# Performance work log

Measured on AMD Instinct MI355X. Metric: run time of the kernel, lower is better.

## Reference

```python
import jax, jax.numpy as jnp
import numpy as np

B, C, LQ, D = 4096, 64, 32, 128
H = 192  # 1.5 * dim
MARGIN = 1.0
EPS = 1e-12


def l2norm(x):
    return x * jax.lax.rsqrt(jnp.maximum(jnp.sum(x * x, axis=1, keepdims=True), EPS))


def setup_inputs() -> dict:
    key = jax.random.key(0)
    ks = jax.random.split(key, 16)
    question_word_embs = jax.random.normal(ks[0], (B, LQ, D), jnp.float32)
    question_lengths = jax.random.randint(ks[1], (B,), 1, LQ + 1, jnp.int32)
    header_embs = jax.random.normal(ks[2], (B, C, D), jnp.float32)
    table_word_embs = jax.random.normal(ks[3], (B, C, D), jnp.float32)
    num_cols = jax.random.randint(ks[4], (B,), 1, C + 1, jnp.int32)
    masks = (jnp.arange(C)[None, :] < num_cols[:, None]).astype(jnp.float32)
    labels = (jax.random.uniform(ks[5], (B,)) < 0.5).astype(jnp.float32)
    # table_encoder_dense: Dense(1.5*dim, relu) -> Dense(dim, relu)
    W1 = jax.random.normal(ks[6], (2 * D, H), jnp.float32) / np.sqrt(2 * D)
    b1 = jnp.zeros((H,), jnp.float32)
    W2 = jax.random.normal(ks[7], (H, D), jnp.float32) / np.sqrt(H)
    b2 = jnp.zeros((D,), jnp.float32)
    # query LSTM(dim, activation='relu'): gate order i, f, c, o (Keras)
    Wx = jax.random.normal(ks[8], (D, 4 * D), jnp.float32) / np.sqrt(D)
    Wh = jax.random.normal(ks[9], (D, 4 * D), jnp.float32) / np.sqrt(D)
    b_lstm = jnp.zeros((4 * D,), jnp.float32)
    return dict(question_word_embs=question_word_embs, question_lengths=question_lengths,
                header_embs=header_embs, table_word_embs=table_word_embs,
                num_cols=num_cols, masks=masks, labels=labels,
                W1=W1, b1=b1, W2=W2, b2=b2, Wx=Wx, Wh=Wh, b_lstm=b_lstm)


def masked_lstm(x, lengths, Wx, Wh, b):
    # x: [B, L, D]; returns final hidden state at each row's true length
    xs = jnp.transpose(x, (1, 0, 2))  # [L, B, D]
    h0 = jnp.zeros((x.shape[0], D), x.dtype)
    c0 = jnp.zeros_like(h0)

    def step(carry, inp):
        h, c = carry
        t, x_t = inp
        z = x_t @ Wx + h @ Wh + b  # [B, 4D]
        i, f, g, o = jnp.split(z, 4, axis=1)
        i = jax.nn.sigmoid(i)
        f = jax.nn.sigmoid(f)
        g = jax.nn.relu(g)           # activation='relu'
        o = jax.nn.sigmoid(o)
        c_new = f * c + i * g
        h_new = o * jax.nn.relu(c_new)
        m = (t < lengths)[:, None].astype(x_t.dtype)
        return (m * h_new + (1 - m) * h, m * c_new + (1 - m) * c), None

    (h, _), _ = jax.lax.scan(step, (h0, c0), (jnp.arange(xs.shape[0]), xs))
    return h


def reference(question_word_embs, question_lengths, header_embs, table_word_embs,
              num_cols, masks, labels, W1, b1, W2, b2, Wx, Wh, b_lstm):
    # ---- table path ----
    flat = jnp.concatenate([header_embs.reshape(-1, D), table_word_embs.reshape(-1, D)], axis=1)  # [B*C, 2D]
    h = jax.nn.relu(flat @ W1 + b1)
    te = jax.nn.relu(h @ W2 + b2).reshape(B, C, D)
    te = te * masks[:, :, None]
    te = jnp.sum(te, axis=1) / num_cols.astype(jnp.float32)[:, None]
    te = l2norm(te)
    # ---- query path (ragged-word LSTM encoder) ----
    qe = masked_lstm(question_word_embs, question_lengths, Wx, Wh, b_lstm)
    qe = l2norm(qe)
    # ---- contrastive loss ----
    d = jnp.sum(jnp.square(qe - te), axis=1)
    d_sqrt = jnp.sqrt(d)
    loss = labels * d + (1.0 - labels) * jnp.square(jnp.maximum(0.0, MARGIN - d_sqrt))
    return 0.5 * jnp.mean(loss)
```

## Files before the change

kernel.cpp:

```cpp
#include <hip/hip_runtime.h>
#include <math.h>

#define B_  4096
#define C_  64
#define LQ_ 32
#define D_  128
#define H_  192

typedef __attribute__((ext_vector_type(8))) short bf16x8;
typedef __attribute__((ext_vector_type(4))) float f32x4;

#define KEEP(x) asm volatile("" : "+v"(x))

__device__ inline unsigned cvt_pk_bf16(float lo, float hi) {
    unsigned r;
    asm("v_cvt_pk_bf16_f32 %0, %1, %2" : "=v"(r) : "v"(lo), "v"(hi));
    return r;
}
__device__ inline short f2b(float x) { return (short)(cvt_pk_bf16(x, x) & 0xffff); }
__device__ inline float sigm(float x) { return 1.f / (1.f + __expf(-x)); }

__device__ inline void wg_barrier() {
    asm volatile("s_waitcnt lgkmcnt(0)" ::: "memory");
    __builtin_amdgcn_s_barrier();
    asm volatile("" ::: "memory");
}

__global__ __launch_bounds__(256) void prep_kernel(
    const float* __restrict__ W1, const float* __restrict__ W2,
    const float* __restrict__ Wx, const float* __restrict__ Wh,
    short* __restrict__ W1T, short* __restrict__ W2T, short* __restrict__ WTl)
{
    int idx = blockIdx.x * 256 + threadIdx.x;
    if (idx < 192 * 256) {
        int j = idx >> 8, k = idx & 255;
        W1T[idx] = f2b(W1[k * H_ + j]);
    }
    if (idx < 128 * 192) {
        int j = idx / 192, k = idx - j * 192;
        W2T[idx] = f2b(W2[k * D_ + j]);
    }
    if (idx < 512 * 256) {
        int p = idx >> 8, k = idx & 255;
        int w = p >> 6, g = (p >> 4) & 3, jj = p & 15;
        int jo = g * 128 + w * 16 + jj;
        float v = (k < 128) ? Wx[k * 512 + jo] : Wh[(k - 128) * 512 + jo];
        WTl[idx] = f2b(v);
    }
}

__global__ __launch_bounds__(256, 2)
void table_kernel(
    const float* __restrict__ header, const float* __restrict__ tword,
    const float* __restrict__ masks, const int* __restrict__ num_cols,
    const short* __restrict__ W1T, const float* __restrict__ b1,
    const short* __restrict__ W2T, const float* __restrict__ b2,
    float* __restrict__ te_out)
{
    const int bb0 = blockIdx.x * 4;
    const int tid = threadIdx.x;
    const int w   = tid >> 6;
    const int l   = tid & 63;
    const int lg  = l >> 4;
    const int ln  = l & 15;

    __shared__ __align__(16) short flat_s[2][16 * 256];
    __shared__ __align__(16) short h_s[16 * 192];
    __shared__ float msk_s[4][64];
    __shared__ float ncol_s[4];
    __shared__ float redv[128];
    __shared__ float redq[2];

    bf16x8 bw1[3][8];
    float bias1[3][4];
    #pragma unroll
    for (int ct = 0; ct < 3; ++ct) {
        int j = w * 48 + ct * 16 + ln;
        #pragma unroll
        for (int ks = 0; ks < 8; ++ks)
            bw1[ct][ks] = *(const bf16x8*)&W1T[j * 256 + ks * 32 + lg * 8];
        #pragma unroll
        for (int reg = 0; reg < 4; ++reg)
            bias1[ct][reg] = b1[w * 48 + ct * 16 + lg * 4 + reg];
    }
    bf16x8 bw2[2][6];
    float bias2[2][4];
    #pragma unroll
    for (int ct = 0; ct < 2; ++ct) {
        int j = w * 32 + ct * 16 + ln;
        #pragma unroll
        for (int ks = 0; ks < 6; ++ks)
            bw2[ct][ks] = *(const bf16x8*)&W2T[j * 192 + ks * 32 + lg * 8];
        #pragma unroll
        for (int reg = 0; reg < 4; ++reg)
            bias2[ct][reg] = b2[w * 32 + ct * 16 + lg * 4 + reg];
    }
    #pragma unroll
    for (int ct = 0; ct < 3; ++ct) {
        #pragma unroll
        for (int ks = 0; ks < 8; ++ks) KEEP(bw1[ct][ks]);
        #pragma unroll
        for (int reg = 0; reg < 4; ++reg) KEEP(bias1[ct][reg]);
    }
    #pragma unroll
    for (int ct = 0; ct < 2; ++ct) {
        #pragma unroll
        for (int ks = 0; ks < 6; ++ks) KEEP(bw2[ct][ks]);
        #pragma unroll
        for (int reg = 0; reg < 4; ++reg) KEEP(bias2[ct][reg]);
    }

    ((float*)msk_s)[tid] = masks[(size_t)bb0 * C_ + tid];
    if (tid < 4) ncol_s[tid] = (float)num_cols[bb0 + tid];
    __syncthreads();

    float4 pf0[4], pf1[4];
    auto issue = [&](int cc, float4 (&dst)[4]) {
        int b    = bb0 + (cc >> 2);
        int row0 = (cc & 3) * 16;
        #pragma unroll
        for (int i = 0; i < 4; ++i) {
            int idx = i * 256 + tid;
            int r   = idx >> 6;
            int c   = idx & 63;
            const float* src = (c < 32)
                ? &header[((size_t)b * C_ + row0 + r) * D_ + c * 4]
                : &tword [((size_t)b * C_ + row0 + r) * D_ + (c - 32) * 4];
            dst[i] = *(const float4*)src;
        }
    };
    issue(0, pf0);
    issue(1, pf1);

    float csum[2][4] = {{0.f, 0.f, 0.f, 0.f}, {0.f, 0.f, 0.f, 0.f}};
    const int row = ln;
    const int swz = (ln & 7) << 4;

    auto body = [&](int cc, float4 (&pfc)[4], char* fbuf) {
        const int bi = cc >> 2;

        #pragma unroll
        for (int i = 0; i < 4; ++i) {
            int idx = i * 256 + tid;
            int r   = idx >> 6;
            int c   = idx & 63;
            uint2 p;
            p.x = cvt_pk_bf16(pfc[i].x, pfc[i].y);
            p.y = cvt_pk_bf16(pfc[i].z, pfc[i].w);
            *(uint2*)(fbuf + r * 512 + ((c * 8) ^ ((r & 7) << 4))) = p;
        }
        if (cc + 2 < 16) issue(cc + 2, pfc);
        wg_barrier();

        {
            f32x4 acc[3];
            #pragma unroll
            for (int ct = 0; ct < 3; ++ct)
                acc[ct] = (f32x4){bias1[ct][0], bias1[ct][1], bias1[ct][2], bias1[ct][3]};
            #pragma unroll
            for (int ks = 0; ks < 8; ++ks) {
                bf16x8 a = *(const bf16x8*)(fbuf + row * 512 + ((ks * 64 + lg * 16) ^ swz));
                #pragma unroll
                for (int ct = 0; ct < 3; ++ct)
                    acc[ct] = __builtin_amdgcn_mfma_f32_16x16x32_bf16(bw1[ct][ks], a, acc[ct], 0, 0, 0);
            }
            #pragma unroll
            for (int ct = 0; ct < 3; ++ct) {
                int col0 = w * 48 + ct * 16 + lg * 4;
                uint2 hp;
                hp.x = cvt_pk_bf16(fmaxf(acc[ct][0], 0.f), fmaxf(acc[ct][1], 0.f));
                hp.y = cvt_pk_bf16(fmaxf(acc[ct][2], 0.f), fmaxf(acc[ct][3], 0.f));
                *(uint2*)((char*)h_s + row * 384 + ((col0 * 2) ^ swz)) = hp;
            }
        }
        wg_barrier();

        {
            f32x4 acc2[2];
            #pragma unroll
            for (int ct = 0; ct < 2; ++ct)
                acc2[ct] = (f32x4){bias2[ct][0], bias2[ct][1], bias2[ct][2], bias2[ct][3]};
            #pragma unroll
            for (int ks = 0; ks < 6; ++ks) {
                bf16x8 a = *(const bf16x8*)((char*)h_s + row * 384 + ((ks * 64 + lg * 16) ^ swz));
                #pragma unroll
                for (int ct = 0; ct < 2; ++ct)
                    acc2[ct] = __builtin_amdgcn_mfma_f32_16x16x32_bf16(bw2[ct][ks], a, acc2[ct], 0, 0, 0);
            }
            float m = msk_s[bi][(cc & 3) * 16 + ln];
            #pragma unroll
            for (int ct = 0; ct < 2; ++ct)
                #pragma unroll
                for (int reg = 0; reg < 4; ++reg)
                    csum[ct][reg] = fmaf(fmaxf(acc2[ct][reg], 0.f), m, csum[ct][reg]);
        }

        if ((cc & 3) == 3) {
            #pragma unroll
            for (int s = 1; s < 16; s <<= 1)
                #pragma unroll
                for (int ct = 0; ct < 2; ++ct)
                    #pragma unroll
                    for (int reg = 0; reg < 4; ++reg)
                        csum[ct][reg] += __shfl_xor(csum[ct][reg], s, 64);
            if (ln == 0) {
                #pragma unroll
                for (int ct = 0; ct < 2; ++ct)
                    #pragma unroll
                    for (int reg = 0; reg < 4; ++reg)
                        redv[w * 32 + ct * 16 + lg * 4 + reg] = csum[ct][reg];
            }
            wg_barrier();
            float v = 0.f;
            if (tid < 128) {
                v = redv[tid] / ncol_s[bi];
                float s2 = v * v;
                #pragma unroll
                for (int sh = 1; sh < 64; sh <<= 1) s2 += __shfl_xor(s2, sh, 64);
                if (l == 0) redq[w] = s2;
            }
            wg_barrier();
            if (tid < 128) {
                float inv = rsqrtf(fmaxf(redq[0] + redq[1], 1e-12f));
                te_out[(size_t)(bb0 + bi) * D_ + tid] = v * inv;
            }
            #pragma unroll
            for (int ct = 0; ct < 2; ++ct)
                #pragma unroll
                for (int reg = 0; reg < 4; ++reg)
                    csum[ct][reg] = 0.f;
        }
    };

    for (int p = 0; p < 8; ++p) {
        body(p * 2,     pf0, (char*)flat_s[0]);
        body(p * 2 + 1, pf1, (char*)flat_s[1]);
    }
}

__global__ __launch_bounds__(512) __attribute__((amdgpu_waves_per_eu(1, 2)))
void lstm_kernel(
    const float* __restrict__ q, const int* __restrict__ lengths,
    const short* __restrict__ WTl, const float* __restrict__ bl,
    float* __restrict__ qe_out)
{
    const int tid = threadIdx.x;
    const int b0  = blockIdx.x * 16;
    const int w   = tid >> 6;
    const int l   = tid & 63;
    const int lg  = l >> 4;
    const int ln  = l & 15;
    const int d0  = w * 16 + lg * 4;

    __shared__ __align__(16) short xh[2][16 * 256];
    __shared__ float red8[8][16];

    bf16x8 wf[4][8];
    #pragma unroll
    for (int g = 0; g < 4; ++g)
        #pragma unroll
        for (int ks = 0; ks < 8; ++ks)
            wf[g][ks] = *(const bf16x8*)&WTl[(w * 64 + g * 16 + ln) * 256 + ks * 32 + lg * 8];
    float bias[4][4];
    #pragma unroll
    for (int g = 0; g < 4; ++g)
        #pragma unroll
        for (int reg = 0; reg < 4; ++reg)
            bias[g][reg] = bl[g * 128 + d0 + reg];
    #pragma unroll
    for (int g = 0; g < 4; ++g) {
        #pragma unroll
        for (int ks = 0; ks < 8; ++ks) KEEP(wf[g][ks]);
        #pragma unroll
        for (int reg = 0; reg < 4; ++reg) KEEP(bias[g][reg]);
    }

    float creg[4] = {0.f, 0.f, 0.f, 0.f};
    float hreg[4] = {0.f, 0.f, 0.f, 0.f};
    const int len = lengths[b0 + ln];
    const int sr = tid >> 5, sc = tid & 31;

    float4 qv = *(const float4*)&q[((size_t)(b0 + sr) * LQ_ + 0) * D_ + sc * 4];

    for (int t = 0; t < LQ_; ++t) {
        char* buf = (char*)xh[t & 1];
        uint2 px; px.x = cvt_pk_bf16(qv.x, qv.y); px.y = cvt_pk_bf16(qv.z, qv.w);
        *(uint2*)(buf + sr * 512 + ((sc * 8) ^ ((sr & 7) << 4))) = px;
        uint2 ph; ph.x = cvt_pk_bf16(hreg[0], hreg[1]); ph.y = cvt_pk_bf16(hreg[2], hreg[3]);
        *(uint2*)(buf + ln * 512 + ((256 + d0 * 2) ^ ((ln & 7) << 4))) = ph;
        if (t + 1 < LQ_)
            qv = *(const float4*)&q[((size_t)(b0 + sr) * LQ_ + (t + 1)) * D_ + sc * 4];
        wg_barrier();

        f32x4 acc[4];
        #pragma unroll
        for (int g = 0; g < 4; ++g)
            acc[g] = (f32x4){bias[g][0], bias[g][1], bias[g][2], bias[g][3]};
        #pragma unroll
        for (int ks = 0; ks < 8; ++ks) {
            bf16x8 xf = *(const bf16x8*)(buf + ln * 512 + ((ks * 64 + lg * 16) ^ ((ln & 7) << 4)));
            #pragma unroll
            for (int g = 0; g < 4; ++g)
                acc[g] = __builtin_amdgcn_mfma_f32_16x16x32_bf16(wf[g][ks], xf, acc[g], 0, 0, 0);
        }

        bool live = (t < len);
        #pragma unroll
        for (int reg = 0; reg < 4; ++reg) {
            float iv = sigm(acc[0][reg]);
            float fv = sigm(acc[1][reg]);
            float gv = fmaxf(acc[2][reg], 0.f);
            float ov = sigm(acc[3][reg]);
            float cn = fmaf(fv, creg[reg], iv * gv);
            float hn = ov * fmaxf(cn, 0.f);
            if (live) { creg[reg] = cn; hreg[reg] = hn; }
        }
    }

    float sq = 0.f;
    #pragma unroll
    for (int reg = 0; reg < 4; ++reg) sq = fmaf(hreg[reg], hreg[reg], sq);
    sq += __shfl_xor(sq, 16, 64);
    sq += __shfl_xor(sq, 32, 64);
    if (l < 16) red8[w][ln] = sq;
    wg_barrier();
    float tot = 0.f;
    #pragma unroll
    for (int ww = 0; ww < 8; ++ww) tot += red8[ww][ln];
    float inv = rsqrtf(fmaxf(tot, 1e-12f));
    float4 o;
    o.x = hreg[0] * inv; o.y = hreg[1] * inv; o.z = hreg[2] * inv; o.w = hreg[3] * inv;
    *(float4*)&qe_out[(size_t)(b0 + ln) * D_ + d0] = o;
}

__global__ __launch_bounds__(64) void loss_kernel(
    const float* __restrict__ te, const float* __restrict__ qe,
    const float* __restrict__ labels, float* __restrict__ partial)
{
    const int tid = threadIdx.x;
    const int b   = blockIdx.x * 64 + tid;
    float dsum = 0.f;
    #pragma unroll 8
    for (int k4 = 0; k4 < 32; ++k4) {
        float4 a = *(const float4*)&qe[(size_t)b * D_ + k4 * 4];
        float4 c = *(const float4*)&te[(size_t)b * D_ + k4 * 4];
        float dx = a.x - c.x, dy = a.y - c.y, dz = a.z - c.z, dw = a.w - c.w;
        dsum += dx * dx + dy * dy + dz * dz + dw * dw;
    }
    float lab = labels[b];
    float ds  = sqrtf(dsum);
    float ml  = fmaxf(0.f, 1.f - ds);
    float loss = lab * dsum + (1.f - lab) * ml * ml;
    #pragma unroll
    for (int s = 32; s > 0; s >>= 1) loss += __shfl_xor(loss, s, 64);
    if (tid == 0) partial[blockIdx.x] = loss;
}

__global__ void final_kernel(const float* __restrict__ partial, float* __restrict__ out)
{
    const int tid = threadIdx.x;
    float v = partial[tid];
    #pragma unroll
    for (int s = 32; s > 0; s >>= 1) v += __shfl_xor(v, s, 64);
    if (tid == 0) out[0] = 0.5f * v / (float)B_;
}

extern "C" void kernel_launch(void* const* d_in, const int* in_sizes, int n_in,
                              void* d_out, int out_size, void* d_ws, size_t ws_size,
                              hipStream_t stream)
{
    const float* q      = (const float*)d_in[0];
    const int*   qlen   = (const int*)d_in[1];
    const float* header = (const float*)d_in[2];
    const float* tword  = (const float*)d_in[3];
    const int*   ncols  = (const int*)d_in[4];
    const float* masks  = (const float*)d_in[5];
    const float* labels = (const float*)d_in[6];
    const float* W1     = (const float*)d_in[7];
    const float* b1     = (const float*)d_in[8];
    const float* W2     = (const float*)d_in[9];
    const float* b2     = (const float*)d_in[10];
    const float* Wx     = (const float*)d_in[11];
    const float* Wh     = (const float*)d_in[12];
    const float* bl     = (const float*)d_in[13];
    float* out = (float*)d_out;

    float* te      = (float*)d_ws;
    float* qe      = te + (size_t)B_ * D_;
    float* partial = qe + (size_t)B_ * D_;
    short* W1T     = (short*)(partial + 64);
    short* W2T     = W1T + 192 * 256;
    short* WTl     = W2T + 128 * 192;

    prep_kernel<<<512, 256, 0, stream>>>(W1, W2, Wx, Wh, W1T, W2T, WTl);
    table_kernel<<<B_ / 4, 256, 0, stream>>>(header, tword, masks, ncols, W1T, b1, W2T, b2, te);
    lstm_kernel<<<B_ / 16, 512, 0, stream>>>(q, qlen, WTl, bl, qe);
    loss_kernel<<<B_ / 64, 64, 0, stream>>>(te, qe, labels, partial);
    final_kernel<<<1, 64, 0, stream>>>(partial, out);
}
```

Measured before the change: 150.8 us.

## Double-buffer hidden tile and defer per-table normalization to cut barriers

The table kernel now double-buffers the hidden-activation tile in shared memory. Staging of the next input chunk moves between the two GEMM stages, so each chunk needs one fewer workgroup barrier. The per-batch reduction and L2 normalization, which used two extra barriers every four chunks, is deferred: partial column sums go into a per-batch shared array and all four batch rows are normalized once at the end. This uses more LDS and changes the prefetch ordering, which may affect occupancy at two blocks per CU.

Result: slower. 191.6 us (+27.1%).

```diff
diff --git a/kernel.cpp b/kernel.cpp
--- a/kernel.cpp
+++ b/kernel.cpp
@@ -65,11 +65,11 @@
     const int ln  = l & 15;
 
     __shared__ __align__(16) short flat_s[2][16 * 256];
-    __shared__ __align__(16) short h_s[16 * 192];
+    __shared__ __align__(16) short h_s2[2][16 * 192];
     __shared__ float msk_s[4][64];
     __shared__ float ncol_s[4];
-    __shared__ float redv[128];
-    __shared__ float redq[2];
+    __shared__ float csum_s[4][128];
+    __shared__ float redq[2][4];
 
     bf16x8 bw1[3][8];
     float bias1[3][4];
@@ -112,7 +112,6 @@
 
     ((float*)msk_s)[tid] = masks[(size_t)bb0 * C_ + tid];
     if (tid < 4) ncol_s[tid] = (float)num_cols[bb0 + tid];
-    __syncthreads();
 
     float4 pf0[4], pf1[4];
     auto issue = [&](int cc, float4 (&dst)[4]) {
@@ -129,16 +128,7 @@
             dst[i] = *(const float4*)src;
         }
     };
-    issue(0, pf0);
-    issue(1, pf1);
-
-    float csum[2][4] = {{0.f, 0.f, 0.f, 0.f}, {0.f, 0.f, 0.f, 0.f}};
-    const int row = ln;
-    const int swz = (ln & 7) << 4;
-
-    auto body = [&](int cc, float4 (&pfc)[4], char* fbuf) {
-        const int bi = cc >> 2;
-
+    auto stage = [&](float4 (&pfc)[4], char* fbuf) {
         #pragma unroll
         for (int i = 0; i < 4; ++i) {
             int idx = i * 256 + tid;
@@ -149,8 +139,24 @@
             p.y = cvt_pk_bf16(pfc[i].z, pfc[i].w);
             *(uint2*)(fbuf + r * 512 + ((c * 8) ^ ((r & 7) << 4))) = p;
         }
-        if (cc + 2 < 16) issue(cc + 2, pfc);
-        wg_barrier();
+    };
+
+    issue(0, pf0);
+    issue(1, pf1);
+    __syncthreads();
+
+    stage(pf0, (char*)flat_s[0]);
+    issue(2, pf0);
+    wg_barrier();
+
+    float csum[2][4] = {{0.f, 0.f, 0.f, 0.f}, {0.f, 0.f, 0.f, 0.f}};
+    const int row = ln;
+    const int swz = (ln & 7) << 4;
+
+    auto body = [&](int cc, float4 (&pfN)[4], bool doStage) {
+        char* fbuf = (char*)flat_s[cc & 1];
+        char* hbuf = (char*)h_s2[cc & 1];
+        const int bi = cc >> 2;
 
         {
             f32x4 acc[3];
@@ -170,9 +176,15 @@
                 uint2 hp;
                 hp.x = cvt_pk_bf16(fmaxf(acc[ct][0], 0.f), fmaxf(acc[ct][1], 0.f));
                 hp.y = cvt_pk_bf16(fmaxf(acc[ct][2], 0.f), fmaxf(acc[ct][3], 0.f));
-                *(uint2*)((char*)h_s + row * 384 + ((col0 * 2) ^ swz)) = hp;
+                *(uint2*)(hbuf + row * 384 + ((col0 * 2) ^ swz)) = hp;
             }
         }
+
+        if (doStage) {
+            stage(pfN, (char*)flat_s[(cc + 1) & 1]);
+            if (cc + 3 < 16) issue(cc + 3, pfN);
+        }
+
         wg_barrier();
 
         {
@@ -182,7 +194,7 @@
                 acc2[ct] = (f32x4){bias2[ct][0], bias2[ct][1], bias2[ct][2], bias2[ct][3]};
             #pragma unroll
             for (int ks = 0; ks < 6; ++ks) {
-                bf16x8 a = *(const bf16x8*)((char*)h_s + row * 384 + ((ks * 64 + lg * 16) ^ swz));
+                bf16x8 a = *(const bf16x8*)(hbuf + row * 384 + ((ks * 64 + lg * 16) ^ swz));
                 #pragma unroll
                 for (int ct = 0; ct < 2; ++ct)
                     acc2[ct] = __builtin_amdgcn_mfma_f32_16x16x32_bf16(bw2[ct][ks], a, acc2[ct], 0, 0, 0);
@@ -208,21 +220,7 @@
                 for (int ct = 0; ct < 2; ++ct)
                     #pragma unroll
                     for (int reg = 0; reg < 4; ++reg)
-                        redv[w * 32 + ct * 16 + lg * 4 + reg] = csum[ct][reg];
-            }
-            wg_barrier();
-            float v = 0.f;
-            if (tid < 128) {
-                v = redv[tid] / ncol_s[bi];
-                float s2 = v * v;
-                #pragma unroll
-                for (int sh = 1; sh < 64; sh <<= 1) s2 += __shfl_xor(s2, sh, 64);
-                if (l == 0) redq[w] = s2;
-            }
-            wg_barrier();
-            if (tid < 128) {
-                float inv = rsqrtf(fmaxf(redq[0] + redq[1], 1e-12f));
-                te_out[(size_t)(bb0 + bi) * D_ + tid] = v * inv;
+                        csum_s[bi][w * 32 + ct * 16 + lg * 4 + reg] = csum[ct][reg];
             }
             #pragma unroll
             for (int ct = 0; ct < 2; ++ct)
@@ -232,9 +230,32 @@
         }
     };
 
+    #pragma unroll 1
     for (int p = 0; p < 8; ++p) {
-        body(p * 2,     pf0, (char*)flat_s[0]);
-        body(p * 2 + 1, pf1, (char*)flat_s[1]);
+        body(p * 2,     pf1, true);
+        body(p * 2 + 1, pf0, p * 2 + 2 < 16);
+    }
+
+    __syncthreads();
+    float vv[4];
+    if (tid < 128) {
+        #pragma unroll
+        for (int bi = 0; bi < 4; ++bi) {
+            float v = csum_s[bi][tid] / ncol_s[bi];
+            vv[bi] = v;
+            float s2 = v * v;
+            #pragma unroll
+            for (int sh = 1; sh < 64; sh <<= 1) s2 += __shfl_xor(s2, sh, 64);
+            if (l == 0) redq[w][bi] = s2;
+        }
+    }
+    __syncthreads();
+    if (tid < 128) {
+        #pragma unroll
+        for (int bi = 0; bi < 4; ++bi) {
+            float inv = rsqrtf(fmaxf(redq[0][bi] + redq[1][bi], 1e-12f));
+            te_out[(size_t)(bb0 + bi) * D_ + tid] = vv[bi] * inv;
+        }
     }
 }
 
```

## Stage table inputs via global_load_lds fp32 and reload W2 per chunk

Applied to the files above, without the earlier changes.

Replaces the register-prefetch plus bf16-convert-to-LDS path in the table kernel with direct global-to-LDS DMA loads of fp32 rows into a double buffer. The bf16 conversion moves to the LDS read side. W2 fragments and bias are reloaded from global memory every chunk instead of being held in registers, which frees VGPRs. The aim is to cut register pressure and the VALU cost of staging, at the price of doubled LDS footprint, extra LDS read traffic and repeated L2 reads of W2.

Result: slower. 166.8 us (+10.6%).

```diff
diff --git a/kernel.cpp b/kernel.cpp
--- a/kernel.cpp
+++ b/kernel.cpp
@@ -22,6 +22,11 @@
 
 __device__ inline void wg_barrier() {
     asm volatile("s_waitcnt lgkmcnt(0)" ::: "memory");
+    __builtin_amdgcn_s_barrier();
+    asm volatile("" ::: "memory");
+}
+__device__ inline void wg_barrier_vm() {
+    asm volatile("s_waitcnt vmcnt(0) lgkmcnt(0)" ::: "memory");
     __builtin_amdgcn_s_barrier();
     asm volatile("" ::: "memory");
 }
@@ -64,7 +69,7 @@
     const int lg  = l >> 4;
     const int ln  = l & 15;
 
-    __shared__ __align__(16) short flat_s[2][16 * 256];
+    __shared__ __align__(16) float flat32[2][16 * 256];
     __shared__ __align__(16) short h_s[16 * 192];
     __shared__ float msk_s[4][64];
     __shared__ float ncol_s[4];
@@ -72,7 +77,7 @@
     __shared__ float redq[2];
 
     bf16x8 bw1[3][8];
-    float bias1[3][4];
+    float  bias1[3][4];
     #pragma unroll
     for (int ct = 0; ct < 3; ++ct) {
         int j = w * 48 + ct * 16 + ln;
@@ -83,86 +88,76 @@
         for (int reg = 0; reg < 4; ++reg)
             bias1[ct][reg] = b1[w * 48 + ct * 16 + lg * 4 + reg];
     }
-    bf16x8 bw2[2][6];
-    float bias2[2][4];
-    #pragma unroll
-    for (int ct = 0; ct < 2; ++ct) {
-        int j = w * 32 + ct * 16 + ln;
-        #pragma unroll
-        for (int ks = 0; ks < 6; ++ks)
-            bw2[ct][ks] = *(const bf16x8*)&W2T[j * 192 + ks * 32 + lg * 8];
-        #pragma unroll
-        for (int reg = 0; reg < 4; ++reg)
-            bias2[ct][reg] = b2[w * 32 + ct * 16 + lg * 4 + reg];
-    }
     #pragma unroll
     for (int ct = 0; ct < 3; ++ct) {
         #pragma unroll
         for (int ks = 0; ks < 8; ++ks) KEEP(bw1[ct][ks]);
         #pragma unroll
         for (int reg = 0; reg < 4; ++reg) KEEP(bias1[ct][reg]);
-    }
-    #pragma unroll
-    for (int ct = 0; ct < 2; ++ct) {
-        #pragma unroll
-        for (int ks = 0; ks < 6; ++ks) KEEP(bw2[ct][ks]);
-        #pragma unroll
-        for (int reg = 0; reg < 4; ++reg) KEEP(bias2[ct][reg]);
     }
 
     ((float*)msk_s)[tid] = masks[(size_t)bb0 * C_ + tid];
     if (tid < 4) ncol_s[tid] = (float)num_cols[bb0 + tid];
-    __syncthreads();
-
-    float4 pf0[4], pf1[4];
-    auto issue = [&](int cc, float4 (&dst)[4]) {
+
+    auto stage_issue = [&](int cc, int buf) {
         int b    = bb0 + (cc >> 2);
         int row0 = (cc & 3) * 16;
         #pragma unroll
         for (int i = 0; i < 4; ++i) {
-            int idx = i * 256 + tid;
-            int r   = idx >> 6;
-            int c   = idx & 63;
-            const float* src = (c < 32)
-                ? &header[((size_t)b * C_ + row0 + r) * D_ + c * 4]
-                : &tword [((size_t)b * C_ + row0 + r) * D_ + (c - 32) * 4];
-            dst[i] = *(const float4*)src;
+            int r = w * 4 + i;
+            int p = ((l * 16) ^ ((r & 7) << 4)) >> 2;
+            const float* srcp = (p < 128)
+                ? header + ((size_t)b * C_ + row0 + r) * D_ + p
+                : tword  + ((size_t)b * C_ + row0 + r) * D_ + (p - 128);
+            __builtin_amdgcn_global_load_lds(
+                (const __attribute__((address_space(1))) unsigned*)srcp,
+                (__attribute__((address_space(3))) unsigned*)&flat32[buf][r * 256],
+                16, 0, 0);
         }
     };
-    issue(0, pf0);
-    issue(1, pf1);
+
+    stage_issue(0, 0);
+    __syncthreads();
 
     float csum[2][4] = {{0.f, 0.f, 0.f, 0.f}, {0.f, 0.f, 0.f, 0.f}};
-    const int row = ln;
     const int swz = (ln & 7) << 4;
 
-    auto body = [&](int cc, float4 (&pfc)[4], char* fbuf) {
-        const int bi = cc >> 2;
-
-        #pragma unroll
-        for (int i = 0; i < 4; ++i) {
-            int idx = i * 256 + tid;
-            int r   = idx >> 6;
-            int c   = idx & 63;
-            uint2 p;
-            p.x = cvt_pk_bf16(pfc[i].x, pfc[i].y);
-            p.y = cvt_pk_bf16(pfc[i].z, pfc[i].w);
-            *(uint2*)(fbuf + r * 512 + ((c * 8) ^ ((r & 7) << 4))) = p;
-        }
-        if (cc + 2 < 16) issue(cc + 2, pfc);
-        wg_barrier();
+    for (int cc = 0; cc < 16; ++cc) {
+        const int bi  = cc >> 2;
+        const int cur = cc & 1;
+
+        bf16x8 w2f[2][6];
+        #pragma unroll
+        for (int ct = 0; ct < 2; ++ct)
+            #pragma unroll
+            for (int ks = 0; ks < 6; ++ks)
+                w2f[ct][ks] = *(const bf16x8*)&W2T[(w * 32 + ct * 16 + ln) * 192 + ks * 32 + lg * 8];
+        float4 b2v[2];
+        #pragma unroll
+        for (int ct = 0; ct < 2; ++ct)
+            b2v[ct] = *(const float4*)&b2[w * 32 + ct * 16 + lg * 4];
+        if (cc + 1 < 16) stage_issue(cc + 1, cur ^ 1);
 
         {
+            const char* fb = (const char*)flat32[cur] + ln * 1024;
             f32x4 acc[3];
             #pragma unroll
             for (int ct = 0; ct < 3; ++ct)
                 acc[ct] = (f32x4){bias1[ct][0], bias1[ct][1], bias1[ct][2], bias1[ct][3]};
             #pragma unroll
             for (int ks = 0; ks < 8; ++ks) {
-                bf16x8 a = *(const bf16x8*)(fbuf + row * 512 + ((ks * 64 + lg * 16) ^ swz));
+                int base = ks * 128 + lg * 32;
+                f32x4 a0 = *(const f32x4*)(fb + ((base)      ^ swz));
+                f32x4 a1 = *(const f32x4*)(fb + ((base + 16) ^ swz));
+                unsigned uu[4];
+                uu[0] = cvt_pk_bf16(a0[0], a0[1]);
+                uu[1] = cvt_pk_bf16(a0[2], a0[3]);
+                uu[2] = cvt_pk_bf16(a1[0], a1[1]);
+                uu[3] = cvt_pk_bf16(a1[2], a1[3]);
+                bf16x8 bfrag = *(bf16x8*)uu;
                 #pragma unroll
                 for (int ct = 0; ct < 3; ++ct)
-                    acc[ct] = __builtin_amdgcn_mfma_f32_16x16x32_bf16(bw1[ct][ks], a, acc[ct], 0, 0, 0);
+                    acc[ct] = __builtin_amdgcn_mfma_f32_16x16x32_bf16(bw1[ct][ks], bfrag, acc[ct], 0, 0, 0);
             }
             #pragma unroll
             for (int ct = 0; ct < 3; ++ct) {
@@ -170,7 +165,7 @@
                 uint2 hp;
                 hp.x = cvt_pk_bf16(fmaxf(acc[ct][0], 0.f), fmaxf(acc[ct][1], 0.f));
                 hp.y = cvt_pk_bf16(fmaxf(acc[ct][2], 0.f), fmaxf(acc[ct][3], 0.f));
-                *(uint2*)((char*)h_s + row * 384 + ((col0 * 2) ^ swz)) = hp;
+                *(uint2*)((char*)h_s + ln * 384 + ((col0 * 2) ^ swz)) = hp;
             }
         }
         wg_barrier();
@@ -179,13 +174,13 @@
             f32x4 acc2[2];
             #pragma unroll
             for (int ct = 0; ct < 2; ++ct)
-                acc2[ct] = (f32x4){bias2[ct][0], bias2[ct][1], bias2[ct][2], bias2[ct][3]};
+                acc2[ct] = (f32x4){b2v[ct].x, b2v[ct].y, b2v[ct].z, b2v[ct].w};
             #pragma unroll
             for (int ks = 0; ks < 6; ++ks) {
-                bf16x8 a = *(const bf16x8*)((char*)h_s + row * 384 + ((ks * 64 + lg * 16) ^ swz));
+                bf16x8 a = *(const bf16x8*)((char*)h_s + ln * 384 + ((ks * 64 + lg * 16) ^ swz));
                 #pragma unroll
                 for (int ct = 0; ct < 2; ++ct)
-                    acc2[ct] = __builtin_amdgcn_mfma_f32_16x16x32_bf16(bw2[ct][ks], a, acc2[ct], 0, 0, 0);
+                    acc2[ct] = __builtin_amdgcn_mfma_f32_16x16x32_bf16(w2f[ct][ks], a, acc2[ct], 0, 0, 0);
             }
             float m = msk_s[bi][(cc & 3) * 16 + ln];
             #pragma unroll
@@ -230,11 +225,8 @@
                 for (int reg = 0; reg < 4; ++reg)
                     csum[ct][reg] = 0.f;
         }
-    };
-
-    for (int p = 0; p < 8; ++p) {
-        body(p * 2,     pf0, (char*)flat_s[0]);
-        body(p * 2 + 1, pf1, (char*)flat_s[1]);
+
+        wg_barrier_vm();
     }
 }
 
```
